# Optimization experiments

Measured on AMD Instinct MI355X. Metric: run time of the kernel, lower is better.

Reference implementation:

```python
import jax, jax.numpy as jnp
import numpy as np

S, B, H = 4096, 32, 512

def setup_inputs() -> dict:
    key = jax.random.key(0)
    k1, k2, k3, k4, k5, k6 = jax.random.split(key, 6)
    sc = 1.0 / np.sqrt(H)
    return {
        "hidden_states": jax.random.normal(k1, (S, B, H), dtype=jnp.float32),
        "Wq": jax.random.normal(k2, (H, H), dtype=jnp.float32) * sc,
        "bq": jax.random.normal(k3, (H,), dtype=jnp.float32) * sc,
        "Wk": jax.random.normal(k4, (H, H), dtype=jnp.float32) * sc,
        "bk": jax.random.normal(k5, (H,), dtype=jnp.float32) * sc,
        "lengths": jax.random.randint(k6, (B,), 1, S + 1, dtype=jnp.int64),
    }

def reference(hidden_states, Wq, bq, Wk, bk, lengths):
    # hidden_states: [S, B, H] (time-first, as in the torch module)
    # query projection then mean over time -> [B, H]
    q = jnp.mean(hidden_states @ Wq.T + bq, axis=0)
    # key: tanh(linear) -> [S, B, H], then batch-first [B, S, H]
    key = jnp.tanh(hidden_states @ Wk.T + bk)
    key_bsh = jnp.transpose(key, (1, 0, 2))
    # attention scores: [B, S]
    scores = jnp.einsum("bsh,bh->bs", key_bsh, q)
    # length mask: positions >= length get -10000 (additive, as in torch code)
    pos = jnp.arange(scores.shape[1])[None, :]
    mask = (pos >= lengths[:, None]).astype(scores.dtype) * -10000.0
    probs = jax.nn.softmax(scores + mask, axis=-1)
    # weighted sum of keys -> [B, H]
    return jnp.einsum("bs,bsh->bh", probs, key_bsh)
```

## Files before the change

### kernel.cpp

```cpp
#include <hip/hip_runtime.h>
#include <hip/hip_bf16.h>
#include <hip/hip_fp16.h>

#define S_LEN 4096
#define B_N   32
#define H_N   512
#define BH    (B_N * H_N)
#define CROWS 64
#define NCH   (S_LEN / CROWS)

typedef __attribute__((ext_vector_type(8))) short bf16x8;
typedef __attribute__((ext_vector_type(4))) float f32x4;

union bfu { __hip_bfloat162 h; unsigned u; };
__device__ __forceinline__ unsigned pk2(float a, float b) {
    bfu x; x.h = __float22bfloat162_rn(make_float2(a, b));
    return x.u;
}

__global__ __launch_bounds__(256) void prep_kernel(const float* __restrict__ hs,
                                                   float* __restrict__ hsum,
                                                   const float* __restrict__ Wk,
                                                   unsigned short* __restrict__ WbF) {
    int bid = blockIdx.x, t = threadIdx.x;
    if (bid < 512) {
        int col = ((bid & 15) * 256 + t) * 4;
        size_t s0 = (size_t)(bid >> 4) * 128;
        float4 acc = {0.f, 0.f, 0.f, 0.f};
        #pragma unroll 8
        for (int i = 0; i < 128; ++i) {
            float4 v = *(const float4*)(hs + (s0 + i) * BH + col);
            acc.x += v.x; acc.y += v.y; acc.z += v.z; acc.w += v.w;
        }
        atomicAdd(&hsum[col],     acc.x);
        atomicAdd(&hsum[col + 1], acc.y);
        atomicAdd(&hsum[col + 2], acc.z);
        atomicAdd(&hsum[col + 3], acc.w);
    } else {
        int slot = (bid - 512) * 256 + t;
        int lane = slot & 63;
        int n    = (slot >> 6) & 3;
        int ks   = (slot >> 8) & 15;
        int wn   = slot >> 12;
        int col = wn * 64 + n * 16 + (lane & 15);
        int k   = ks * 32 + (lane >> 4) * 8;
        const float* src = Wk + (size_t)col * H_N + k;
        float4 v0 = *(const float4*)(src);
        float4 v1 = *(const float4*)(src + 4);
        uint4 u4 = { pk2(v0.x, v0.y), pk2(v0.z, v0.w),
                     pk2(v1.x, v1.y), pk2(v1.z, v1.w) };
        *(uint4*)(WbF + (size_t)slot * 8) = u4;
    }
}

__global__ __launch_bounds__(512) void q_kernel(const float* __restrict__ hsum,
                                                const float* __restrict__ Wq,
                                                const float* __restrict__ bq,
                                                float* __restrict__ q) {
    int b = blockIdx.x, part = blockIdx.y, t = threadIdx.x;
    int lane = t & 63, wv = t >> 6;
    __shared__ float hrow[H_N];
    hrow[t] = hsum[b * H_N + t] * (1.f / S_LEN);
    __syncthreads();
    float h0 = hrow[lane * 8 + 0], h1 = hrow[lane * 8 + 1];
    float h2 = hrow[lane * 8 + 2], h3 = hrow[lane * 8 + 3];
    float h4 = hrow[lane * 8 + 4], h5 = hrow[lane * 8 + 5];
    float h6 = hrow[lane * 8 + 6], h7 = hrow[lane * 8 + 7];
    #pragma unroll
    for (int j = 0; j < 8; ++j) {
        int h = part * 64 + wv * 8 + j;
        const float* wrow = Wq + (size_t)h * H_N + lane * 8;
        float4 w0 = *(const float4*)(wrow);
        float4 w1 = *(const float4*)(wrow + 4);
        float acc = h0 * w0.x + h1 * w0.y + h2 * w0.z + h3 * w0.w
                  + h4 * w1.x + h5 * w1.y + h6 * w1.z + h7 * w1.w;
        acc += __shfl_xor(acc, 1);  acc += __shfl_xor(acc, 2);
        acc += __shfl_xor(acc, 4);  acc += __shfl_xor(acc, 8);
        acc += __shfl_xor(acc, 16); acc += __shfl_xor(acc, 32);
        if (lane == 0) q[b * H_N + h] = acc + bq[h];
    }
}

__global__ __launch_bounds__(512, 4) void fused_kernel(
    const float* __restrict__ hs, const unsigned short* __restrict__ WbF,
    const float* __restrict__ bk, const float* __restrict__ qv,
    const int* __restrict__ lengths,
    float* __restrict__ pm, float* __restrict__ pl, float* __restrict__ po)
{
    int blk = blockIdx.x;
    int b = blk & 31;
    int chunk = blk >> 5;
    int s0 = chunk * CROWS;
    int t = threadIdx.x;

    int len = lengths[b];
    if (s0 >= len) {
        if (t == 0) pm[b * NCH + chunk] = -1e30f;
        return;
    }

    int lane = t & 63, wn = t >> 6;
    int l15 = lane & 15, lg = lane >> 4;

    __shared__ __align__(16) unsigned short A_s[CROWS * H_N];
    __shared__ float q_s[H_N];
    __shared__ float bk_s[H_N];
    __shared__ float scp[8][CROWS];
    __shared__ float p_s[CROWS];

    q_s[t]  = qv[b * H_N + t];
    bk_s[t] = bk[t];

    const float* hb = hs + ((size_t)s0 * B_N + b) * H_N;
    int kq  = t & 127;
    int r0l = t >> 7;
    #pragma unroll 8
    for (int j = 0; j < 16; ++j) {
        int row = r0l + 4 * j;
        float4 v = *(const float4*)(hb + (size_t)row * BH + kq * 4);
        uint2 u2 = { pk2(v.x, v.y), pk2(v.z, v.w) };
        *(uint2*)((char*)A_s + row * 1024 + ((kq * 8) ^ ((row & 7) << 4))) = u2;
    }
    __syncthreads();

    const unsigned short* wbF = WbF + (size_t)wn * 32768 + lane * 8;
    const char* Ab = (const char*)A_s + l15 * 1024;
    int axor = (l15 & 7) << 4;

    f32x4 acc[4][4];
    #pragma unroll
    for (int m = 0; m < 4; ++m)
        #pragma unroll
        for (int n = 0; n < 4; ++n) acc[m][n] = (f32x4){0.f, 0.f, 0.f, 0.f};

    #pragma unroll
    for (int ks = 0; ks < 16; ++ks) {
        const unsigned short* wk = wbF + ks * 2048;
        bf16x8 b0 = *(const bf16x8*)(wk + 0 * 512);
        bf16x8 b1 = *(const bf16x8*)(wk + 1 * 512);
        bf16x8 b2 = *(const bf16x8*)(wk + 2 * 512);
        bf16x8 b3 = *(const bf16x8*)(wk + 3 * 512);
        int off = (ks * 64 + lg * 16) ^ axor;
        bf16x8 a0 = *(const bf16x8*)(Ab + off);
        bf16x8 a1 = *(const bf16x8*)(Ab + 16 * 1024 + off);
        bf16x8 a2 = *(const bf16x8*)(Ab + 32 * 1024 + off);
        bf16x8 a3 = *(const bf16x8*)(Ab + 48 * 1024 + off);
        acc[0][0] = __builtin_amdgcn_mfma_f32_16x16x32_bf16(a0, b0, acc[0][0], 0, 0, 0);
        acc[1][0] = __builtin_amdgcn_mfma_f32_16x16x32_bf16(a1, b0, acc[1][0], 0, 0, 0);
        acc[2][0] = __builtin_amdgcn_mfma_f32_16x16x32_bf16(a2, b0, acc[2][0], 0, 0, 0);
        acc[3][0] = __builtin_amdgcn_mfma_f32_16x16x32_bf16(a3, b0, acc[3][0], 0, 0, 0);
        acc[0][1] = __builtin_amdgcn_mfma_f32_16x16x32_bf16(a0, b1, acc[0][1], 0, 0, 0);
        acc[1][1] = __builtin_amdgcn_mfma_f32_16x16x32_bf16(a1, b1, acc[1][1], 0, 0, 0);
        acc[2][1] = __builtin_amdgcn_mfma_f32_16x16x32_bf16(a2, b1, acc[2][1], 0, 0, 0);
        acc[3][1] = __builtin_amdgcn_mfma_f32_16x16x32_bf16(a3, b1, acc[3][1], 0, 0, 0);
        acc[0][2] = __builtin_amdgcn_mfma_f32_16x16x32_bf16(a0, b2, acc[0][2], 0, 0, 0);
        acc[1][2] = __builtin_amdgcn_mfma_f32_16x16x32_bf16(a1, b2, acc[1][2], 0, 0, 0);
        acc[2][2] = __builtin_amdgcn_mfma_f32_16x16x32_bf16(a2, b2, acc[2][2], 0, 0, 0);
        acc[3][2] = __builtin_amdgcn_mfma_f32_16x16x32_bf16(a3, b2, acc[3][2], 0, 0, 0);
        acc[0][3] = __builtin_amdgcn_mfma_f32_16x16x32_bf16(a0, b3, acc[0][3], 0, 0, 0);
        acc[1][3] = __builtin_amdgcn_mfma_f32_16x16x32_bf16(a1, b3, acc[1][3], 0, 0, 0);
        acc[2][3] = __builtin_amdgcn_mfma_f32_16x16x32_bf16(a2, b3, acc[2][3], 0, 0, 0);
        acc[3][3] = __builtin_amdgcn_mfma_f32_16x16x32_bf16(a3, b3, acc[3][3], 0, 0, 0);
    }

    float sp[4][4] = {{0,0,0,0},{0,0,0,0},{0,0,0,0},{0,0,0,0}};
    #pragma unroll
    for (int m = 0; m < 4; ++m)
        #pragma unroll
        for (int n = 0; n < 4; ++n) {
            int c = wn * 64 + n * 16 + l15;
            float bkv = bk_s[c], qc = q_s[c];
            #pragma unroll
            for (int i = 0; i < 4; ++i) {
                float z = acc[m][n][i] + bkv;
                float e = __expf(2.f * z);
                float kv = 1.f - 2.f * __builtin_amdgcn_rcpf(e + 1.f);
                acc[m][n][i] = kv;
                sp[m][i] = fmaf(kv, qc, sp[m][i]);
            }
        }
    #pragma unroll
    for (int m = 0; m < 4; ++m)
        #pragma unroll
        for (int i = 0; i < 4; ++i) {
            float v = sp[m][i];
            v += __shfl_xor(v, 1); v += __shfl_xor(v, 2);
            v += __shfl_xor(v, 4); v += __shfl_xor(v, 8);
            if (l15 == 0) scp[wn][m * 16 + lg * 4 + i] = v;
        }
    __syncthreads();

    {
        float sc = 0.f;
        #pragma unroll
        for (int w = 0; w < 8; ++w) sc += scp[w][lane];
        if (s0 + lane >= len) sc -= 10000.f;
        float mx = sc;
        #pragma unroll
        for (int d = 1; d < 64; d <<= 1) mx = fmaxf(mx, __shfl_xor(mx, d));
        float p = __expf(sc - mx);
        if (wn == 0) {
            p_s[lane] = p;
            float l = p;
            #pragma unroll
            for (int d = 1; d < 64; d <<= 1) l += __shfl_xor(l, d);
            if (lane == 0) { pm[b * NCH + chunk] = mx; pl[b * NCH + chunk] = l; }
        }
    }
    __syncthreads();

    float o4[4] = {0, 0, 0, 0};
    #pragma unroll
    for (int m = 0; m < 4; ++m)
        #pragma unroll
        for (int i = 0; i < 4; ++i) {
            float p = p_s[m * 16 + lg * 4 + i];
            #pragma unroll
            for (int n = 0; n < 4; ++n) o4[n] = fmaf(p, acc[m][n][i], o4[n]);
        }
    #pragma unroll
    for (int n = 0; n < 4; ++n) {
        float v = o4[n];
        v += __shfl_xor(v, 16);
        v += __shfl_xor(v, 32);
        o4[n] = v;
    }
    if (lg == 0) {
        float* pob = po + ((size_t)b * NCH + chunk) * H_N + wn * 64 + l15;
        #pragma unroll
        for (int n = 0; n < 4; ++n) pob[n * 16] = o4[n];
    }
}

__global__ __launch_bounds__(512) void combine_kernel(
    const float* __restrict__ pm, const float* __restrict__ pl,
    const float* __restrict__ po, float* __restrict__ out)
{
    int b = blockIdx.x, t = threadIdx.x;
    float M = -1e30f;
    #pragma unroll 8
    for (int c = 0; c < NCH; ++c) M = fmaxf(M, pm[b * NCH + c]);
    float den = 0.f, n0 = 0.f;
    #pragma unroll 8
    for (int c = 0; c < NCH; ++c) {
        float w = __expf(pm[b * NCH + c] - M);
        den = fmaf(w, pl[b * NCH + c], den);
        n0  = fmaf(w, po[(size_t)(b * NCH + c) * H_N + t], n0);
    }
    out[b * H_N + t] = n0 / den;
}

extern "C" void kernel_launch(void* const* d_in, const int* in_sizes, int n_in,
                              void* d_out, int out_size, void* d_ws, size_t ws_size,
                              hipStream_t stream) {
    const float* hs      = (const float*)d_in[0];
    const float* Wq      = (const float*)d_in[1];
    const float* bq      = (const float*)d_in[2];
    const float* Wk      = (const float*)d_in[3];
    const float* bk      = (const float*)d_in[4];
    const int*   lengths = (const int*)d_in[5];
    float* out = (float*)d_out;

    float* ws   = (float*)d_ws;
    float* hsum = ws;
    float* qv   = hsum + BH;
    float* pm   = qv + BH;
    float* pl   = pm + B_N * NCH;
    float* po   = pl + B_N * NCH;
    unsigned short* WbF = (unsigned short*)(po + (size_t)B_N * NCH * H_N);

    hipMemsetAsync(hsum, 0, BH * sizeof(float), stream);
    hipLaunchKernelGGL(prep_kernel, dim3(640), dim3(256), 0, stream, hs, hsum, Wk, (unsigned short*)WbF);
    hipLaunchKernelGGL(q_kernel, dim3(B_N, 8), dim3(512), 0, stream, hsum, Wq, bq, qv);
    hipLaunchKernelGGL(fused_kernel, dim3(B_N * NCH), dim3(512), 0, stream,
                       hs, WbF, bk, qv, lengths, pm, pl, po);
    hipLaunchKernelGGL(combine_kernel, dim3(B_N), dim3(512), 0, stream, pm, pl, po, out);
}
```

Before: 179.7 us.

## Stream Wk tiles through LDS with double-buffered async global_load_lds

Replaces the direct per-iteration global loads of the bf16 weight fragments with asynchronous global-to-LDS loads into a per-wave double buffer, prefetching two k-steps ahead and gating on vmcnt/lgkmcnt waits. The goal is to hide weight-load latency behind the MFMA chain. It adds 64 KB of shared memory per block and lowers the launch-bounds occupancy hint from 4 to 2, so fewer blocks can be resident per CU. The hand-written waitcnt counts also interact with the earlier hidden-state global loads, which makes correctness and ordering fragile.

```diff
diff --git a/kernel.cpp b/kernel.cpp
--- a/kernel.cpp
+++ b/kernel.cpp
@@ -16,6 +16,12 @@
 __device__ __forceinline__ unsigned pk2(float a, float b) {
     bfu x; x.h = __float22bfloat162_rn(make_float2(a, b));
     return x.u;
+}
+
+__device__ __forceinline__ void gload_lds16(const void* g, void* l) {
+    __builtin_amdgcn_global_load_lds(
+        (__attribute__((address_space(1))) void*)g,
+        (__attribute__((address_space(3))) void*)l, 16, 0, 0);
 }
 
 __global__ __launch_bounds__(256) void prep_kernel(const float* __restrict__ hs,
@@ -81,7 +87,7 @@
     }
 }
 
-__global__ __launch_bounds__(512, 4) void fused_kernel(
+__global__ __launch_bounds__(512, 2) void fused_kernel(
     const float* __restrict__ hs, const unsigned short* __restrict__ WbF,
     const float* __restrict__ bk, const float* __restrict__ qv,
     const int* __restrict__ lengths,
@@ -103,10 +109,21 @@
     int l15 = lane & 15, lg = lane >> 4;
 
     __shared__ __align__(16) unsigned short A_s[CROWS * H_N];
+    __shared__ __align__(16) unsigned short Bls[8 * 2 * 2048];
     __shared__ float q_s[H_N];
     __shared__ float bk_s[H_N];
     __shared__ float scp[8][CROWS];
     __shared__ float p_s[CROWS];
+
+    const char* wbW = (const char*)WbF + (size_t)wn * 65536 + lane * 16;
+    char* blsW = (char*)Bls + wn * 8192;
+
+    #pragma unroll
+    for (int n = 0; n < 4; ++n)
+        gload_lds16(wbW + 0 * 4096 + n * 1024, blsW + 0 * 4096 + n * 1024);
+    #pragma unroll
+    for (int n = 0; n < 4; ++n)
+        gload_lds16(wbW + 1 * 4096 + n * 1024, blsW + 1 * 4096 + n * 1024);
 
     q_s[t]  = qv[b * H_N + t];
     bk_s[t] = bk[t];
@@ -123,7 +140,6 @@
     }
     __syncthreads();
 
-    const unsigned short* wbF = WbF + (size_t)wn * 32768 + lane * 8;
     const char* Ab = (const char*)A_s + l15 * 1024;
     int axor = (l15 & 7) << 4;
 
@@ -135,16 +151,25 @@
 
     #pragma unroll
     for (int ks = 0; ks < 16; ++ks) {
-        const unsigned short* wk = wbF + ks * 2048;
-        bf16x8 b0 = *(const bf16x8*)(wk + 0 * 512);
-        bf16x8 b1 = *(const bf16x8*)(wk + 1 * 512);
-        bf16x8 b2 = *(const bf16x8*)(wk + 2 * 512);
-        bf16x8 b3 = *(const bf16x8*)(wk + 3 * 512);
+        if (ks == 15) asm volatile("s_waitcnt vmcnt(0)" ::: "memory");
+        else          asm volatile("s_waitcnt vmcnt(4)" ::: "memory");
+        const char* bb = blsW + (ks & 1) * 4096 + lane * 16;
+        bf16x8 b0 = *(const bf16x8*)(bb + 0 * 1024);
+        bf16x8 b1 = *(const bf16x8*)(bb + 1 * 1024);
+        bf16x8 b2 = *(const bf16x8*)(bb + 2 * 1024);
+        bf16x8 b3 = *(const bf16x8*)(bb + 3 * 1024);
         int off = (ks * 64 + lg * 16) ^ axor;
         bf16x8 a0 = *(const bf16x8*)(Ab + off);
         bf16x8 a1 = *(const bf16x8*)(Ab + 16 * 1024 + off);
         bf16x8 a2 = *(const bf16x8*)(Ab + 32 * 1024 + off);
         bf16x8 a3 = *(const bf16x8*)(Ab + 48 * 1024 + off);
+        asm volatile("s_waitcnt lgkmcnt(0)" ::: "memory");
+        if (ks + 2 < 16) {
+            #pragma unroll
+            for (int n = 0; n < 4; ++n)
+                gload_lds16(wbW + (ks + 2) * 4096 + n * 1024,
+                            blsW + (ks & 1) * 4096 + n * 1024);
+        }
         acc[0][0] = __builtin_amdgcn_mfma_f32_16x16x32_bf16(a0, b0, acc[0][0], 0, 0, 0);
         acc[1][0] = __builtin_amdgcn_mfma_f32_16x16x32_bf16(a1, b0, acc[1][0], 0, 0, 0);
         acc[2][0] = __builtin_amdgcn_mfma_f32_16x16x32_bf16(a2, b0, acc[2][0], 0, 0, 0);
```

Measured after the change: 195.8 us. 1.09x slower.

## Fuse time-sum into key GEMM pass and stash fp16 keys for later scoring

Applied to the files above, without the earlier changes.

Removes the separate pass over hidden_states that computed the per-batch time sum. The GEMM kernel now accumulates that sum while staging its tile, and writes tanh(key) tiles as packed fp16 to a workspace buffer. A new score kernel reloads those keys after q is computed and does the masked softmax and weighted sum. This avoids reading the 256MB input twice, at the cost of writing and re-reading a key buffer (roughly 128MB fp16 round trip), an extra launch, and fp16 rounding of the keys.

```diff
diff --git a/kernel.cpp b/kernel.cpp
--- a/kernel.cpp
+++ b/kernel.cpp
@@ -17,111 +17,75 @@
     bfu x; x.h = __float22bfloat162_rn(make_float2(a, b));
     return x.u;
 }
-
-__global__ __launch_bounds__(256) void prep_kernel(const float* __restrict__ hs,
-                                                   float* __restrict__ hsum,
-                                                   const float* __restrict__ Wk,
-                                                   unsigned short* __restrict__ WbF) {
-    int bid = blockIdx.x, t = threadIdx.x;
-    if (bid < 512) {
-        int col = ((bid & 15) * 256 + t) * 4;
-        size_t s0 = (size_t)(bid >> 4) * 128;
-        float4 acc = {0.f, 0.f, 0.f, 0.f};
-        #pragma unroll 8
-        for (int i = 0; i < 128; ++i) {
-            float4 v = *(const float4*)(hs + (s0 + i) * BH + col);
-            acc.x += v.x; acc.y += v.y; acc.z += v.z; acc.w += v.w;
-        }
-        atomicAdd(&hsum[col],     acc.x);
-        atomicAdd(&hsum[col + 1], acc.y);
-        atomicAdd(&hsum[col + 2], acc.z);
-        atomicAdd(&hsum[col + 3], acc.w);
-    } else {
-        int slot = (bid - 512) * 256 + t;
-        int lane = slot & 63;
-        int n    = (slot >> 6) & 3;
-        int ks   = (slot >> 8) & 15;
-        int wn   = slot >> 12;
-        int col = wn * 64 + n * 16 + (lane & 15);
-        int k   = ks * 32 + (lane >> 4) * 8;
-        const float* src = Wk + (size_t)col * H_N + k;
-        float4 v0 = *(const float4*)(src);
-        float4 v1 = *(const float4*)(src + 4);
-        uint4 u4 = { pk2(v0.x, v0.y), pk2(v0.z, v0.w),
-                     pk2(v1.x, v1.y), pk2(v1.z, v1.w) };
-        *(uint4*)(WbF + (size_t)slot * 8) = u4;
-    }
-}
-
-__global__ __launch_bounds__(512) void q_kernel(const float* __restrict__ hsum,
-                                                const float* __restrict__ Wq,
-                                                const float* __restrict__ bq,
-                                                float* __restrict__ q) {
-    int b = blockIdx.x, part = blockIdx.y, t = threadIdx.x;
-    int lane = t & 63, wv = t >> 6;
-    __shared__ float hrow[H_N];
-    hrow[t] = hsum[b * H_N + t] * (1.f / S_LEN);
-    __syncthreads();
-    float h0 = hrow[lane * 8 + 0], h1 = hrow[lane * 8 + 1];
-    float h2 = hrow[lane * 8 + 2], h3 = hrow[lane * 8 + 3];
-    float h4 = hrow[lane * 8 + 4], h5 = hrow[lane * 8 + 5];
-    float h6 = hrow[lane * 8 + 6], h7 = hrow[lane * 8 + 7];
-    #pragma unroll
-    for (int j = 0; j < 8; ++j) {
-        int h = part * 64 + wv * 8 + j;
-        const float* wrow = Wq + (size_t)h * H_N + lane * 8;
-        float4 w0 = *(const float4*)(wrow);
-        float4 w1 = *(const float4*)(wrow + 4);
-        float acc = h0 * w0.x + h1 * w0.y + h2 * w0.z + h3 * w0.w
-                  + h4 * w1.x + h5 * w1.y + h6 * w1.z + h7 * w1.w;
-        acc += __shfl_xor(acc, 1);  acc += __shfl_xor(acc, 2);
-        acc += __shfl_xor(acc, 4);  acc += __shfl_xor(acc, 8);
-        acc += __shfl_xor(acc, 16); acc += __shfl_xor(acc, 32);
-        if (lane == 0) q[b * H_N + h] = acc + bq[h];
-    }
-}
-
-__global__ __launch_bounds__(512, 4) void fused_kernel(
+union hfu { __half2 h; unsigned u; };
+__device__ __forceinline__ unsigned pkh(float a, float b) {
+    hfu x; x.h = __floats2half2_rn(a, b);
+    return x.u;
+}
+__device__ __forceinline__ float2 uph(unsigned u) {
+    hfu x; x.u = u; return __half22float2(x.h);
+}
+
+__global__ __launch_bounds__(256) void wkfrag_kernel(const float* __restrict__ Wk,
+                                                     unsigned short* __restrict__ WbF) {
+    int slot = blockIdx.x * 256 + threadIdx.x;
+    int lane = slot & 63;
+    int n    = (slot >> 6) & 3;
+    int ks   = (slot >> 8) & 15;
+    int wn   = slot >> 12;
+    int col = wn * 64 + n * 16 + (lane & 15);
+    int k   = ks * 32 + (lane >> 4) * 8;
+    const float* src = Wk + (size_t)col * H_N + k;
+    float4 v0 = *(const float4*)(src);
+    float4 v1 = *(const float4*)(src + 4);
+    uint4 u4 = { pk2(v0.x, v0.y), pk2(v0.z, v0.w),
+                 pk2(v1.x, v1.y), pk2(v1.z, v1.w) };
+    *(uint4*)(WbF + (size_t)slot * 8) = u4;
+}
+
+__global__ __launch_bounds__(512, 4) void gemm_kernel(
     const float* __restrict__ hs, const unsigned short* __restrict__ WbF,
-    const float* __restrict__ bk, const float* __restrict__ qv,
-    const int* __restrict__ lengths,
-    float* __restrict__ pm, float* __restrict__ pl, float* __restrict__ po)
+    const float* __restrict__ bk, const int* __restrict__ lengths,
+    float* __restrict__ hsum, unsigned* __restrict__ keyw)
 {
     int blk = blockIdx.x;
     int b = blk & 31;
     int chunk = blk >> 5;
     int s0 = chunk * CROWS;
     int t = threadIdx.x;
-
     int len = lengths[b];
-    if (s0 >= len) {
-        if (t == 0) pm[b * NCH + chunk] = -1e30f;
-        return;
-    }
+    bool active = (s0 < len);
 
     int lane = t & 63, wn = t >> 6;
     int l15 = lane & 15, lg = lane >> 4;
 
     __shared__ __align__(16) unsigned short A_s[CROWS * H_N];
-    __shared__ float q_s[H_N];
+    __shared__ float hsred[4][H_N];
     __shared__ float bk_s[H_N];
-    __shared__ float scp[8][CROWS];
-    __shared__ float p_s[CROWS];
-
-    q_s[t]  = qv[b * H_N + t];
+
     bk_s[t] = bk[t];
 
     const float* hb = hs + ((size_t)s0 * B_N + b) * H_N;
     int kq  = t & 127;
     int r0l = t >> 7;
+    float4 cs = {0.f, 0.f, 0.f, 0.f};
     #pragma unroll 8
     for (int j = 0; j < 16; ++j) {
         int row = r0l + 4 * j;
         float4 v = *(const float4*)(hb + (size_t)row * BH + kq * 4);
-        uint2 u2 = { pk2(v.x, v.y), pk2(v.z, v.w) };
-        *(uint2*)((char*)A_s + row * 1024 + ((kq * 8) ^ ((row & 7) << 4))) = u2;
-    }
-    __syncthreads();
+        cs.x += v.x; cs.y += v.y; cs.z += v.z; cs.w += v.w;
+        if (active) {
+            uint2 u2 = { pk2(v.x, v.y), pk2(v.z, v.w) };
+            *(uint2*)((char*)A_s + row * 1024 + ((kq * 8) ^ ((row & 7) << 4))) = u2;
+        }
+    }
+    *(float4*)&hsred[r0l][kq * 4] = cs;
+    __syncthreads();
+    {
+        float s = hsred[0][t] + hsred[1][t] + hsred[2][t] + hsred[3][t];
+        atomicAdd(&hsum[b * H_N + t], s);
+    }
+    if (!active) return;
 
     const unsigned short* wbF = WbF + (size_t)wn * 32768 + lane * 8;
     const char* Ab = (const char*)A_s + l15 * 1024;
@@ -163,21 +127,104 @@
         acc[3][3] = __builtin_amdgcn_mfma_f32_16x16x32_bf16(a3, b3, acc[3][3], 0, 0, 0);
     }
 
-    float sp[4][4] = {{0,0,0,0},{0,0,0,0},{0,0,0,0},{0,0,0,0}};
+    unsigned kw[32];
     #pragma unroll
     for (int m = 0; m < 4; ++m)
         #pragma unroll
         for (int n = 0; n < 4; ++n) {
-            int c = wn * 64 + n * 16 + l15;
-            float bkv = bk_s[c], qc = q_s[c];
+            float bkv = bk_s[wn * 64 + n * 16 + l15];
+            float kv[4];
             #pragma unroll
             for (int i = 0; i < 4; ++i) {
                 float z = acc[m][n][i] + bkv;
                 float e = __expf(2.f * z);
-                float kv = 1.f - 2.f * __builtin_amdgcn_rcpf(e + 1.f);
-                acc[m][n][i] = kv;
-                sp[m][i] = fmaf(kv, qc, sp[m][i]);
+                kv[i] = 1.f - 2.f * __builtin_amdgcn_rcpf(e + 1.f);
             }
+            kw[(m * 4 + n) * 2 + 0] = pkh(kv[0], kv[1]);
+            kw[(m * 4 + n) * 2 + 1] = pkh(kv[2], kv[3]);
+        }
+    uint4* dst = (uint4*)(keyw + (size_t)blk * 16384 + t * 32);
+    #pragma unroll
+    for (int j = 0; j < 8; ++j) dst[j] = ((uint4*)kw)[j];
+}
+
+__global__ __launch_bounds__(512) void q_kernel(const float* __restrict__ hsum,
+                                                const float* __restrict__ Wq,
+                                                const float* __restrict__ bq,
+                                                float* __restrict__ q) {
+    int b = blockIdx.x, part = blockIdx.y, t = threadIdx.x;
+    int lane = t & 63, wv = t >> 6;
+    __shared__ float hrow[H_N];
+    hrow[t] = hsum[b * H_N + t] * (1.f / S_LEN);
+    __syncthreads();
+    float h0 = hrow[lane * 8 + 0], h1 = hrow[lane * 8 + 1];
+    float h2 = hrow[lane * 8 + 2], h3 = hrow[lane * 8 + 3];
+    float h4 = hrow[lane * 8 + 4], h5 = hrow[lane * 8 + 5];
+    float h6 = hrow[lane * 8 + 6], h7 = hrow[lane * 8 + 7];
+    #pragma unroll
+    for (int j = 0; j < 8; ++j) {
+        int h = part * 64 + wv * 8 + j;
+        const float* wrow = Wq + (size_t)h * H_N + lane * 8;
+        float4 w0 = *(const float4*)(wrow);
+        float4 w1 = *(const float4*)(wrow + 4);
+        float acc = h0 * w0.x + h1 * w0.y + h2 * w0.z + h3 * w0.w
+                  + h4 * w1.x + h5 * w1.y + h6 * w1.z + h7 * w1.w;
+        acc += __shfl_xor(acc, 1);  acc += __shfl_xor(acc, 2);
+        acc += __shfl_xor(acc, 4);  acc += __shfl_xor(acc, 8);
+        acc += __shfl_xor(acc, 16); acc += __shfl_xor(acc, 32);
+        if (lane == 0) q[b * H_N + h] = acc + bq[h];
+    }
+}
+
+__global__ __launch_bounds__(512, 4) void score_kernel(
+    const unsigned* __restrict__ keyw, const float* __restrict__ qv,
+    const int* __restrict__ lengths,
+    float* __restrict__ pm, float* __restrict__ pl, float* __restrict__ po)
+{
+    int blk = blockIdx.x;
+    int b = blk & 31;
+    int chunk = blk >> 5;
+    int s0 = chunk * CROWS;
+    int t = threadIdx.x;
+    int len = lengths[b];
+    if (s0 >= len) {
+        if (t == 0) pm[b * NCH + chunk] = -1e30f;
+        return;
+    }
+    int lane = t & 63, wn = t >> 6;
+    int l15 = lane & 15, lg = lane >> 4;
+
+    __shared__ float q_s[H_N];
+    __shared__ float scp[8][CROWS];
+    __shared__ float p_s[CROWS];
+
+    q_s[t] = qv[b * H_N + t];
+
+    unsigned kw[32];
+    const uint4* src = (const uint4*)(keyw + (size_t)blk * 16384 + t * 32);
+    #pragma unroll
+    for (int j = 0; j < 8; ++j) ((uint4*)kw)[j] = src[j];
+    float kvf[4][4][4];
+    #pragma unroll
+    for (int m = 0; m < 4; ++m)
+        #pragma unroll
+        for (int n = 0; n < 4; ++n) {
+            float2 f01 = uph(kw[(m * 4 + n) * 2 + 0]);
+            float2 f23 = uph(kw[(m * 4 + n) * 2 + 1]);
+            kvf[m][n][0] = f01.x; kvf[m][n][1] = f01.y;
+            kvf[m][n][2] = f23.x; kvf[m][n][3] = f23.y;
+        }
+    __syncthreads();
+
+    float sp[4][4] = {{0,0,0,0},{0,0,0,0},{0,0,0,0},{0,0,0,0}};
+    #pragma unroll
+    for (int m = 0; m < 4; ++m)
+        #pragma unroll
+        for (int n = 0; n < 4; ++n) {
+            float qc = q_s[wn * 64 + n * 16 + l15];
+            #pragma unroll
+            for (int i = 0; i < 4; ++i)
+                sp[m][i] = fmaf(kvf[m][n][i], qc, sp[m][i]);
         }
     #pragma unroll
     for (int m = 0; m < 4; ++m)
@@ -216,7 +263,7 @@
         for (int i = 0; i < 4; ++i) {
             float p = p_s[m * 16 + lg * 4 + i];
             #pragma unroll
-            for (int n = 0; n < 4; ++n) o4[n] = fmaf(p, acc[m][n][i], o4[n]);
+            for (int n = 0; n < 4; ++n) o4[n] = fmaf(p, kvf[m][n][i], o4[n]);
         }
     #pragma unroll
     for (int n = 0; n < 4; ++n) {
@@ -268,11 +315,14 @@
     float* pl   = pm + B_N * NCH;
     float* po   = pl + B_N * NCH;
     unsigned short* WbF = (unsigned short*)(po + (size_t)B_N * NCH * H_N);
+    unsigned* keyw = (unsigned*)(WbF + (size_t)H_N * H_N);
 
     hipMemsetAsync(hsum, 0, BH * sizeof(float), stream);
-    hipLaunchKernelGGL(prep_kernel, dim3(640), dim3(256), 0, stream, hs, hsum, Wk, (unsigned short*)WbF);
+    hipLaunchKernelGGL(wkfrag_kernel, dim3(128), dim3(256), 0, stream, Wk, WbF);
+    hipLaunchKernelGGL(gemm_kernel, dim3(B_N * NCH), dim3(512), 0, stream,
+                       hs, WbF, bk, lengths, hsum, keyw);
     hipLaunchKernelGGL(q_kernel, dim3(B_N, 8), dim3(512), 0, stream, hsum, Wq, bq, qv);
-    hipLaunchKernelGGL(fused_kernel, dim3(B_N * NCH), dim3(512), 0, stream,
-                       hs, WbF, bk, qv, lengths, pm, pl, po);
+    hipLaunchKernelGGL(score_kernel, dim3(B_N * NCH), dim3(512), 0, stream,
+                       keyw, qv, lengths, pm, pl, po);
     hipLaunchKernelGGL(combine_kernel, dim3(B_N), dim3(512), 0, stream, pm, pl, po, out);
 }
```

New measurement: 181.8 us. About the same (+1.1%).

## Convert hidden states to bf16 once in prep pass, reuse in fused kernel

Applied to the files above, without the earlier changes.

The prep kernel now reads each (batch, chunk) tile of hidden states a single time. From that read it computes the column sums for the query mean and, for tiles inside the valid length, writes a bf16 copy to a workspace buffer. The fused kernel then loads this half-size bf16 tile instead of re-reading the fp32 input and converting it. This removes a second fp32 read of the active rows, at the cost of an extra bf16 write and read through the workspace and more atomics on hsum.

```diff
diff --git a/kernel.cpp b/kernel.cpp
--- a/kernel.cpp
+++ b/kernel.cpp
@@ -21,23 +21,35 @@
 __global__ __launch_bounds__(256) void prep_kernel(const float* __restrict__ hs,
                                                    float* __restrict__ hsum,
                                                    const float* __restrict__ Wk,
-                                                   unsigned short* __restrict__ WbF) {
+                                                   unsigned short* __restrict__ WbF,
+                                                   unsigned short* __restrict__ AT,
+                                                   const int* __restrict__ lengths) {
     int bid = blockIdx.x, t = threadIdx.x;
-    if (bid < 512) {
-        int col = ((bid & 15) * 256 + t) * 4;
-        size_t s0 = (size_t)(bid >> 4) * 128;
-        float4 acc = {0.f, 0.f, 0.f, 0.f};
+    if (bid < 2048) {
+        int b = bid & 31, chunk = bid >> 5;
+        int s0 = chunk * CROWS;
+        bool active = (s0 < lengths[b]);
+        const float* hb = hs + ((size_t)s0 * B_N + b) * H_N;
+        unsigned short* at = AT + (size_t)bid * (CROWS * H_N);
+        int kq = t & 127, rg = t >> 7;
+        float4 cs = {0.f, 0.f, 0.f, 0.f};
+        __shared__ float hsred[2][H_N];
         #pragma unroll 8
-        for (int i = 0; i < 128; ++i) {
-            float4 v = *(const float4*)(hs + (s0 + i) * BH + col);
-            acc.x += v.x; acc.y += v.y; acc.z += v.z; acc.w += v.w;
-        }
-        atomicAdd(&hsum[col],     acc.x);
-        atomicAdd(&hsum[col + 1], acc.y);
-        atomicAdd(&hsum[col + 2], acc.z);
-        atomicAdd(&hsum[col + 3], acc.w);
+        for (int j = 0; j < 32; ++j) {
+            int row = rg + 2 * j;
+            float4 v = *(const float4*)(hb + (size_t)row * BH + kq * 4);
+            cs.x += v.x; cs.y += v.y; cs.z += v.z; cs.w += v.w;
+            if (active) {
+                uint2 u2 = { pk2(v.x, v.y), pk2(v.z, v.w) };
+                *(uint2*)(at + row * H_N + kq * 4) = u2;
+            }
+        }
+        *(float4*)&hsred[rg][kq * 4] = cs;
+        __syncthreads();
+        atomicAdd(&hsum[b * H_N + t],       hsred[0][t]       + hsred[1][t]);
+        atomicAdd(&hsum[b * H_N + t + 256], hsred[0][t + 256] + hsred[1][t + 256]);
     } else {
-        int slot = (bid - 512) * 256 + t;
+        int slot = (bid - 2048) * 256 + t;
         int lane = slot & 63;
         int n    = (slot >> 6) & 3;
         int ks   = (slot >> 8) & 15;
@@ -82,7 +94,7 @@
 }
 
 __global__ __launch_bounds__(512, 4) void fused_kernel(
-    const float* __restrict__ hs, const unsigned short* __restrict__ WbF,
+    const unsigned short* __restrict__ AT, const unsigned short* __restrict__ WbF,
     const float* __restrict__ bk, const float* __restrict__ qv,
     const int* __restrict__ lengths,
     float* __restrict__ pm, float* __restrict__ pl, float* __restrict__ po)
@@ -111,15 +123,13 @@
     q_s[t]  = qv[b * H_N + t];
     bk_s[t] = bk[t];
 
-    const float* hb = hs + ((size_t)s0 * B_N + b) * H_N;
-    int kq  = t & 127;
-    int r0l = t >> 7;
-    #pragma unroll 8
-    for (int j = 0; j < 16; ++j) {
-        int row = r0l + 4 * j;
-        float4 v = *(const float4*)(hb + (size_t)row * BH + kq * 4);
-        uint2 u2 = { pk2(v.x, v.y), pk2(v.z, v.w) };
-        *(uint2*)((char*)A_s + row * 1024 + ((kq * 8) ^ ((row & 7) << 4))) = u2;
+    const unsigned short* at = AT + (size_t)blk * (CROWS * H_N);
+    int co = t & 63, rg8 = t >> 6;
+    #pragma unroll
+    for (int j = 0; j < 8; ++j) {
+        int row = rg8 + 8 * j;
+        uint4 v = *(const uint4*)(at + row * H_N + co * 8);
+        *(uint4*)((char*)A_s + row * 1024 + ((co * 16) ^ ((row & 7) << 4))) = v;
     }
     __syncthreads();
 
@@ -268,11 +278,13 @@
     float* pl   = pm + B_N * NCH;
     float* po   = pl + B_N * NCH;
     unsigned short* WbF = (unsigned short*)(po + (size_t)B_N * NCH * H_N);
+    unsigned short* AT  = WbF + (size_t)H_N * H_N;
 
     hipMemsetAsync(hsum, 0, BH * sizeof(float), stream);
-    hipLaunchKernelGGL(prep_kernel, dim3(640), dim3(256), 0, stream, hs, hsum, Wk, (unsigned short*)WbF);
+    hipLaunchKernelGGL(prep_kernel, dim3(2176), dim3(256), 0, stream,
+                       hs, hsum, Wk, WbF, AT, lengths);
     hipLaunchKernelGGL(q_kernel, dim3(B_N, 8), dim3(512), 0, stream, hsum, Wq, bq, qv);
     hipLaunchKernelGGL(fused_kernel, dim3(B_N * NCH), dim3(512), 0, stream,
-                       hs, WbF, bk, qv, lengths, pm, pl, po);
+                       AT, WbF, bk, qv, lengths, pm, pl, po);
     hipLaunchKernelGGL(combine_kernel, dim3(B_N), dim3(512), 0, stream, pm, pl, po, out);
 }
```

Result: slower. 183.7 us (+2.2%).
